# Performance work log

Measured on AMD Instinct MI355X. Metric: run time of the kernel, lower is better.

The kernel has to match this reference:

```python
import jax, jax.numpy as jnp
import numpy as np

N = 100000      # number of rows/cols (square sparse matrix)
NNZ = 1600000   # number of nonzeros
D = 64          # feature dim


def setup_inputs() -> dict:
    key = jax.random.key(0)
    k1, k2, k3, k4 = jax.random.split(key, 4)
    x = jax.random.normal(k1, (N, D), dtype=jnp.float32)
    row = jax.random.randint(k2, (NNZ,), 0, N, dtype=jnp.int64)
    col = jax.random.randint(k3, (NNZ,), 0, N, dtype=jnp.int64)
    value = jax.random.uniform(k4, (NNZ,), dtype=jnp.float32)
    return {"x": x, "row": row, "col": col, "value": value, "size": N}


def reference(x, row, col, value, size):
    # y[row[i]] += value[i] * x[col[i]]  (COO SpMM via segment-sum scatter-add)
    gathered = value[:, None] * x[col]                 # [NNZ, D]
    y = jax.ops.segment_sum(gathered, row, num_segments=size)  # [size, D]
    return y
```

## Files before the change

kernel.cpp:

```cpp
#include <hip/hip_runtime.h>
#include <hip/hip_bf16.h>


#define D 64

__global__ __launch_bounds__(256) void spmm_scatter_kernel(
    const float* __restrict__ x,
    const int* __restrict__ row,
    const int* __restrict__ col,
    const float* __restrict__ value,
    float* __restrict__ y,
    int nnz) {
  int gid  = blockIdx.x * blockDim.x + threadIdx.x;
  int lane = gid & (D - 1);
  int i    = gid >> 6;
  if (i >= nnz) return;

  int   r = row[i];
  int   c = col[i];
  float v = value[i];

  float xv = x[(size_t)c * D + lane];
  atomicAdd(&y[(size_t)r * D + lane], v * xv);
}

extern "C" void kernel_launch(void* const* d_in, const int* in_sizes, int n_in,
                              void* d_out, int out_size, void* d_ws, size_t ws_size,
                              hipStream_t stream) {
  const float* x     = (const float*)d_in[0];
  const int*   row   = (const int*)d_in[1];
  const int*   col   = (const int*)d_in[2];
  const float* value = (const float*)d_in[3];

  float* y  = (float*)d_out;
  int    nnz = in_sizes[1];

  hipMemsetAsync(y, 0, (size_t)out_size * sizeof(float), stream);

  long long total_threads = (long long)nnz * D;
  int block = 256;
  int grid  = (int)((total_threads + block - 1) / block);
  spmm_scatter_kernel<<<grid, block, 0, stream>>>(x, row, col, value, y, nnz);
}
```

Baseline: 432.3 us.

## Convert COO to CSR on device and reduce rows without atomics

Replaces the per-element atomic scatter-add with a device-side COO-to-CSR conversion: a row histogram, a single-block prefix scan, and a scatter of (col, value) pairs into row-sorted order. A row-parallel kernel then accumulates each output row in registers and writes it once, removing the 64 float atomics per nonzero. The cost is several extra kernels, including a single-block 1024-thread scan over 100k rows that may serialize, plus atomics on a 100k-entry histogram and cursor. The old atomic path is kept as a fallback when the workspace is too small.

Result: slower. 650.5 us (+50.5%).

```diff
diff --git a/kernel.cpp b/kernel.cpp
--- a/kernel.cpp
+++ b/kernel.cpp
@@ -1,27 +1,79 @@
 #include <hip/hip_runtime.h>
-#include <hip/hip_bf16.h>
 
 
 #define D 64
 
 __global__ __launch_bounds__(256) void spmm_scatter_kernel(
-    const float* __restrict__ x,
-    const int* __restrict__ row,
-    const int* __restrict__ col,
-    const float* __restrict__ value,
-    float* __restrict__ y,
-    int nnz) {
-  int gid  = blockIdx.x * blockDim.x + threadIdx.x;
-  int lane = gid & (D - 1);
-  int i    = gid >> 6;
+    const float* __restrict__ x, const int* __restrict__ row,
+    const int* __restrict__ col, const float* __restrict__ value,
+    float* __restrict__ y, int nnz) {
+  long long gid = (long long)blockIdx.x * blockDim.x + threadIdx.x;
+  int lane = (int)(gid & (D - 1));
+  long long i = gid >> 6;
   if (i >= nnz) return;
+  int r = row[i]; int c = col[i]; float v = value[i];
+  atomicAdd(&y[(size_t)r * D + lane], v * x[(size_t)c * D + lane]);
+}
 
-  int   r = row[i];
-  int   c = col[i];
-  float v = value[i];
+__global__ __launch_bounds__(256) void hist_kernel(
+    const int* __restrict__ row, unsigned* __restrict__ hist, int nnz) {
+  int i = blockIdx.x * blockDim.x + threadIdx.x;
+  if (i < nnz) atomicAdd(&hist[row[i]], 1u);
+}
 
-  float xv = x[(size_t)c * D + lane];
-  atomicAdd(&y[(size_t)r * D + lane], v * xv);
+__global__ __launch_bounds__(1024) void scan_kernel(
+    unsigned* __restrict__ a, unsigned* __restrict__ cursor, int n, int nnz) {
+  const int tid = threadIdx.x;
+  const int chunk = (n + 1023) >> 10;
+  int lo = tid * chunk;
+  int hi = lo + chunk; if (hi > n) hi = n;
+  if (lo > n) lo = n;
+  unsigned s = 0;
+  for (int k = lo; k < hi; ++k) s += a[k];
+  __shared__ unsigned part[1024];
+  part[tid] = s;
+  __syncthreads();
+  for (int off = 1; off < 1024; off <<= 1) {
+    unsigned t = (tid >= off) ? part[tid - off] : 0u;
+    __syncthreads();
+    part[tid] += t;
+    __syncthreads();
+  }
+  unsigned run = (tid == 0) ? 0u : part[tid - 1];
+  for (int k = lo; k < hi; ++k) {
+    unsigned h = a[k];
+    a[k] = run;
+    cursor[k] = run;
+    run += h;
+  }
+  if (tid == 0) a[n] = (unsigned)nnz;
+}
+
+__global__ __launch_bounds__(256) void scatter_kernel(
+    const int* __restrict__ row, const int* __restrict__ col,
+    const float* __restrict__ value, unsigned* __restrict__ cursor,
+    int2* __restrict__ pairs, int nnz) {
+  int i = blockIdx.x * blockDim.x + threadIdx.x;
+  if (i >= nnz) return;
+  int r = row[i];
+  unsigned dst = atomicAdd(&cursor[r], 1u);
+  pairs[dst] = make_int2(col[i], __float_as_int(value[i]));
+}
+
+__global__ __launch_bounds__(256) void reduce_kernel(
+    const float* __restrict__ x, const unsigned* __restrict__ row_start,
+    const int2* __restrict__ pairs, float* __restrict__ y, int n) {
+  long long gid = (long long)blockIdx.x * blockDim.x + threadIdx.x;
+  int lane = (int)(gid & (D - 1));
+  long long r = gid >> 6;
+  if (r >= n) return;
+  unsigned s = row_start[r], e = row_start[r + 1];
+  float acc = 0.f;
+  for (unsigned j = s; j < e; ++j) {
+    int2 p = pairs[j];
+    acc += __int_as_float(p.y) * x[(size_t)p.x * D + lane];
+  }
+  y[(size_t)r * D + lane] = acc;
 }
 
 extern "C" void kernel_launch(void* const* d_in, const int* in_sizes, int n_in,
@@ -31,14 +83,31 @@
   const int*   row   = (const int*)d_in[1];
   const int*   col   = (const int*)d_in[2];
   const float* value = (const float*)d_in[3];
+  float* y   = (float*)d_out;
+  int    nnz = in_sizes[1];
+  int    n   = out_size / D;
 
-  float* y  = (float*)d_out;
-  int    nnz = in_sizes[1];
+  size_t need = (size_t)nnz * 8 + (size_t)(n + 1) * 4 + (size_t)n * 4;
+  if (ws_size < need) {
+    hipMemsetAsync(y, 0, (size_t)out_size * sizeof(float), stream);
+    long long tot = (long long)nnz * D;
+    spmm_scatter_kernel<<<(int)((tot + 255) / 256), 256, 0, stream>>>(
+        x, row, col, value, y, nnz);
+    return;
+  }
 
-  hipMemsetAsync(y, 0, (size_t)out_size * sizeof(float), stream);
+  char* ws = (char*)d_ws;
+  int2*     pairs  = (int2*)ws;
+  unsigned* rs     = (unsigned*)(ws + (size_t)nnz * 8);
+  unsigned* cursor = rs + (n + 1);
 
-  long long total_threads = (long long)nnz * D;
-  int block = 256;
-  int grid  = (int)((total_threads + block - 1) / block);
-  spmm_scatter_kernel<<<grid, block, 0, stream>>>(x, row, col, value, y, nnz);
+  hipMemsetAsync(rs, 0, (size_t)(n + 1) * sizeof(unsigned), stream);
+
+  int blocks_nnz = (nnz + 255) / 256;
+  hist_kernel<<<blocks_nnz, 256, 0, stream>>>(row, rs, nnz);
+  scan_kernel<<<1, 1024, 0, stream>>>(rs, cursor, n, nnz);
+  scatter_kernel<<<blocks_nnz, 256, 0, stream>>>(row, col, value, cursor, pairs, nnz);
+
+  long long tot = (long long)n * D;
+  reduce_kernel<<<(int)((tot + 255) / 256), 256, 0, stream>>>(x, rs, pairs, y, n);
 }
```
